# Optimization experiments

Hardware: AMD Instinct MI355X
Metric: run time of the kernel (lower is better)

Reference implementation:

```python
import jax, jax.numpy as jnp
import numpy as np

DIM = 768
HEADS = 12
SCALE = DIM ** -0.5  # NOTE: module scales by full dim, not head dim


def setup_inputs() -> dict:
    key = jax.random.key(0)
    ks = jax.random.split(key, 5)
    B, N, C = 8, 1024, DIM
    x = jax.random.normal(ks[0], (B, N, C), dtype=jnp.float32)
    W_qkv = jax.random.normal(ks[1], (C, 3 * C), dtype=jnp.float32) * (C ** -0.5)
    b_qkv = jnp.zeros((3 * C,), dtype=jnp.float32)
    W_out = jax.random.normal(ks[2], (C, C), dtype=jnp.float32) * (C ** -0.5)
    b_out = jnp.zeros((C,), dtype=jnp.float32)
    return {"x": x, "W_qkv": W_qkv, "b_qkv": b_qkv, "W_out": W_out, "b_out": b_out}


def reference(x, W_qkv, b_qkv, W_out, b_out) -> jnp.ndarray:
    B, N, C = x.shape
    H, D = HEADS, C // HEADS
    qkv = x @ W_qkv + b_qkv                       # [B, N, 3C]
    q, k, v = jnp.split(qkv, 3, axis=-1)
    # [B, N, C] -> [B, H, N, D]
    q = q.reshape(B, N, H, D).transpose(0, 2, 1, 3)
    k = k.reshape(B, N, H, D).transpose(0, 2, 1, 3)
    v = v.reshape(B, N, H, D).transpose(0, 2, 1, 3)
    attn = jnp.einsum("bhnd,bhmd->bhnm", q, k) * SCALE
    attn = jax.nn.softmax(attn, axis=-1)
    out = jnp.einsum("bhnm,bhmd->bhnd", attn, v)   # [B, H, N, D]
    out = out.transpose(0, 2, 1, 3).reshape(B, N, C)
    return out @ W_out + b_out
```

## Files before the change

kernel.cpp:

```cpp
#include <hip/hip_runtime.h>
#include <hip/hip_bf16.h>

typedef __attribute__((ext_vector_type(4))) float f32x4;
typedef __attribute__((ext_vector_type(4))) unsigned u32x4;
typedef __attribute__((ext_vector_type(8))) short bf16x8;

#define SCALE_F 0.03608439182435161f
#define QSCALE  (0.03608439182435161f * 1.44269504088896f)

__device__ __forceinline__ unsigned short f2bf(float f) {
    union { float f; unsigned u; } v; v.f = f;
    return (unsigned short)((v.u + 0x7FFFu + ((v.u >> 16) & 1u)) >> 16);
}

__device__ __forceinline__ float fast_exp2(float x) {
#if __has_builtin(__builtin_amdgcn_exp2f)
    return __builtin_amdgcn_exp2f(x);
#else
    return exp2f(x);
#endif
}

__device__ __forceinline__ void gload_lds16(const void* g, void* l) {
    __builtin_amdgcn_global_load_lds(
        (const __attribute__((address_space(1))) unsigned int*)g,
        (__attribute__((address_space(3))) unsigned int*)l, 16, 0, 0);
}

__global__ __launch_bounds__(256) void xcvt_kernel(const float* __restrict__ X,
                                                   unsigned short* __restrict__ Xb,
                                                   int n8) {
    const int i = blockIdx.x * 256 + threadIdx.x;
    if (i < n8) {
        f32x4 a = *(const f32x4*)(X + (size_t)i * 8);
        f32x4 b = *(const f32x4*)(X + (size_t)i * 8 + 4);
        bf16x8 w;
#pragma unroll
        for (int j = 0; j < 4; ++j) { w[j] = (short)f2bf(a[j]); w[4 + j] = (short)f2bf(b[j]); }
        *(bf16x8*)(Xb + (size_t)i * 8) = w;
    }
}

__global__ __launch_bounds__(256) void wtrans_kernel(const float* __restrict__ W,
                                                     unsigned short* __restrict__ WT,
                                                     int R, int C) {
    __shared__ unsigned short T[64][68];
    const int t = threadIdx.x;
    const int r0 = blockIdx.y * 64, c0 = blockIdx.x * 64;
    {
        const int lr = t >> 4, lc = (t & 15) * 4;
#pragma unroll
        for (int p = 0; p < 4; ++p) {
            const float* s = W + (size_t)(r0 + lr + p * 16) * C + c0 + lc;
            f32x4 v = *(const f32x4*)s;
            unsigned short* d = &T[lr + p * 16][lc];
            d[0] = f2bf(v[0]); d[1] = f2bf(v[1]); d[2] = f2bf(v[2]); d[3] = f2bf(v[3]);
        }
    }
    __syncthreads();
    {
        const int oc = t >> 3, j0 = (t & 7) * 8;
#pragma unroll
        for (int p = 0; p < 2; ++p) {
            const int c = oc + p * 32;
            bf16x8 v;
#pragma unroll
            for (int j = 0; j < 8; ++j) v[j] = (short)T[j0 + j][c];
            *(bf16x8*)(WT + (size_t)(c0 + c) * R + r0 + j0) = v;
        }
    }
}

__global__ __launch_bounds__(256) void qkv_gemm_kernel(
    const unsigned short* __restrict__ Xb, const unsigned short* __restrict__ WT,
    const float* __restrict__ bias,
    unsigned short* __restrict__ Qw, unsigned short* __restrict__ Kw,
    unsigned short* __restrict__ VTw)
{
    __shared__ unsigned short Alds[128 * 32];
    __shared__ unsigned short Blds[128 * 32];

    const int t = threadIdx.x;
    const int lane = t & 63, wave = t >> 6;
    const int l15 = lane & 15, l4 = lane >> 4;
    const int m0 = blockIdx.x * 128, n0 = blockIdx.y * 128;
    const int wr = wave >> 1, wc = wave & 1;

    f32x4 acc[4][4];
#pragma unroll
    for (int m = 0; m < 4; ++m)
#pragma unroll
        for (int n = 0; n < 4; ++n) acc[m][n] = (f32x4){0.f, 0.f, 0.f, 0.f};

    for (int k0 = 0; k0 < 768; k0 += 32) {
#pragma unroll
        for (int c = 0; c < 2; ++c) {
            const int o = wave * 1024 + lane * 16 + c * 4096;
            const int row = o >> 6, cb = o & 63;
            gload_lds16((const char*)(Xb + (size_t)(m0 + row) * 768 + k0) + cb,
                        (char*)Alds + wave * 1024 + c * 4096);
            gload_lds16((const char*)(WT + (size_t)(n0 + row) * 768 + k0) + cb,
                        (char*)Blds + wave * 1024 + c * 4096);
        }
        __syncthreads();
        bf16x8 af[4], bfr[4];
#pragma unroll
        for (int m = 0; m < 4; ++m)
            af[m] = *(const bf16x8*)((const char*)Alds + (wr * 64 + m * 16 + l15) * 64 + l4 * 16);
#pragma unroll
        for (int n = 0; n < 4; ++n)
            bfr[n] = *(const bf16x8*)((const char*)Blds + (wc * 64 + n * 16 + l15) * 64 + l4 * 16);
#pragma unroll
        for (int m = 0; m < 4; ++m)
#pragma unroll
            for (int n = 0; n < 4; ++n)
                acc[m][n] = __builtin_amdgcn_mfma_f32_16x16x32_bf16(af[m], bfr[n], acc[m][n], 0, 0, 0);
        __syncthreads();
    }

#pragma unroll
    for (int n = 0; n < 4; ++n) {
        const int col = n0 + wc * 64 + n * 16 + l15;
        const float bv = bias[col];
        const int which = col / 768;
        const int cc = col - which * 768;
        const int h = cc >> 6, dd = cc & 63;
#pragma unroll
        for (int m = 0; m < 4; ++m) {
#pragma unroll
            for (int r = 0; r < 4; ++r) {
                const int row = m0 + wr * 64 + m * 16 + l4 * 4 + r;
                const int b = row >> 10, ntok = row & 1023;
                const size_t bh = (size_t)b * 12 + h;
                float val = acc[m][n][r] + bv;
                if (which == 0) val *= QSCALE;
                const unsigned short hv = f2bf(val);
                if (which == 0)      Qw[(bh * 1024 + ntok) * 64 + dd] = hv;
                else if (which == 1) Kw[(bh * 1024 + ntok) * 64 + dd] = hv;
                else                 VTw[(bh * 64 + dd) * 1024 + ntok] = hv;
            }
        }
    }
}

__global__ __launch_bounds__(256) void attn_kernel(
    const unsigned short* __restrict__ Qw, const unsigned short* __restrict__ Kw,
    const unsigned short* __restrict__ VTw, unsigned short* __restrict__ A2)
{
    __shared__ unsigned short Klds[2 * 64 * 64];
    __shared__ unsigned short Vlds[2 * 64 * 64];
    __shared__ float Flds[4 * 16];

    const int t = threadIdx.x, lane = t & 63, wave = t >> 6;
    const int l15 = lane & 15, l4 = lane >> 4;
    const int wg = (blockIdx.x & 7) * 192 + (blockIdx.x >> 3);
    const int qt = wg & 15, bh = wg >> 4;
    const int q0 = qt * 64;

    const size_t kvbase = (size_t)bh * 1024 * 64;
    const size_t vtbase = (size_t)bh * 64 * 1024;

    const unsigned short* qptr = Qw + kvbase + (size_t)(q0 + wave * 16 + l15) * 64;
    const bf16x8 qf0 = *(const bf16x8*)((const char*)qptr + l4 * 16);
    const bf16x8 qf1 = *(const bf16x8*)((const char*)qptr + 64 + l4 * 16);

    f32x4 oacc[4];
#pragma unroll
    for (int d = 0; d < 4; ++d) oacc[d] = (f32x4){0.f, 0.f, 0.f, 0.f};
    float m_run = -1e30f, l_run = 0.f;

    auto STAGE = [&](int kt, int bufi) {
        const int kv0 = kt * 64;
        char* kb = (char*)Klds + bufi * 8192;
        char* vb = (char*)Vlds + bufi * 8192;
#pragma unroll
        for (int c = 0; c < 2; ++c) {
            const int oo = wave * 1024 + lane * 16 + c * 4096;
            const int R = oo >> 7, w = oo & 127;
            const int sw = w ^ ((R & 7) << 4);
            const int kvs = (R & 0x23) | ((R & 0x0C) << 1) | ((R & 0x10) >> 2);
            gload_lds16((const char*)(Kw + kvbase + (size_t)(kv0 + kvs) * 64) + sw,
                        kb + wave * 1024 + c * 4096);
            gload_lds16((const char*)(VTw + vtbase + (size_t)R * 1024 + kv0) + sw,
                        vb + wave * 1024 + c * 4096);
        }
    };

    STAGE(0, 0);
    for (int kt = 0; kt < 16; ++kt) {
        const int cur = kt & 1;
        if (kt < 15) {
            STAGE(kt + 1, cur ^ 1);
            asm volatile("s_waitcnt vmcnt(4)" ::: "memory");
        } else {
            asm volatile("s_waitcnt vmcnt(0)" ::: "memory");
        }
        __builtin_amdgcn_s_barrier();
        __builtin_amdgcn_sched_barrier(0);
        const char* kb = (const char*)Klds + cur * 8192;
        const char* vb = (const char*)Vlds + cur * 8192;

        f32x4 sacc[4];
#pragma unroll
        for (int i = 0; i < 4; ++i) sacc[i] = (f32x4){0.f, 0.f, 0.f, 0.f};
        __builtin_amdgcn_s_setprio(1);
#pragma unroll
        for (int ks = 0; ks < 2; ++ks) {
            const bf16x8 qq = ks ? qf1 : qf0;
#pragma unroll
            for (int kvf = 0; kvf < 4; ++kvf) {
                const int row = kvf * 16 + l15;
                int addr = row * 128 + ks * 64 + l4 * 16;
                addr ^= (row & 7) << 4;
                const bf16x8 kf = *(const bf16x8*)(kb + addr);
                sacc[kvf] = __builtin_amdgcn_mfma_f32_16x16x32_bf16(kf, qq, sacc[kvf], 0, 0, 0);
            }
        }
        __builtin_amdgcn_s_setprio(0);

        float p[16];
        float tmax = -1e30f;
#pragma unroll
        for (int i = 0; i < 4; ++i)
#pragma unroll
            for (int r = 0; r < 4; ++r) {
                p[i * 4 + r] = sacc[i][r];
                tmax = fmaxf(tmax, sacc[i][r]);
            }
        tmax = fmaxf(tmax, __shfl_xor(tmax, 16));
        tmax = fmaxf(tmax, __shfl_xor(tmax, 32));

        if (!__all(tmax - m_run <= 8.f)) {
            const float mnew = fmaxf(m_run, tmax);
            const float alpha = fast_exp2(m_run - mnew);
            m_run = mnew;
            if (lane < 16) Flds[wave * 16 + lane] = alpha;
            const f32x4 av = *(const f32x4*)(&Flds[wave * 16 + l4 * 4]);
#pragma unroll
            for (int d = 0; d < 4; ++d)
#pragma unroll
                for (int r = 0; r < 4; ++r) oacc[d][r] *= av[r];
            l_run *= alpha;
        }

        float tsum = 0.f;
#pragma unroll
        for (int i = 0; i < 16; ++i) { p[i] = fast_exp2(p[i] - m_run); tsum += p[i]; }
        tsum += __shfl_xor(tsum, 16);
        tsum += __shfl_xor(tsum, 32);
        l_run += tsum;

        bf16x8 paf[2];
#pragma unroll
        for (int ks = 0; ks < 2; ++ks) {
            union { u32x4 u; bf16x8 h; } cv;
#pragma unroll
            for (int j2 = 0; j2 < 4; ++j2)
                asm("v_cvt_pk_bf16_f32 %0, %1, %2"
                    : "=v"(cv.u[j2]) : "v"(p[ks * 8 + 2 * j2]), "v"(p[ks * 8 + 2 * j2 + 1]));
            paf[ks] = cv.h;
        }

        __builtin_amdgcn_s_setprio(1);
#pragma unroll
        for (int ks = 0; ks < 2; ++ks) {
#pragma unroll
            for (int df = 0; df < 4; ++df) {
                const int d = df * 16 + l15;
                int addr = d * 128 + ks * 64 + l4 * 16;
                addr ^= (d & 7) << 4;
                const bf16x8 vf = *(const bf16x8*)(vb + addr);
                oacc[df] = __builtin_amdgcn_mfma_f32_16x16x32_bf16(paf[ks], vf, oacc[df], 0, 0, 0);
            }
        }
        __builtin_amdgcn_s_setprio(0);
        __builtin_amdgcn_s_barrier();
    }

    if (lane < 16) Flds[wave * 16 + lane] = 1.f / l_run;
    const f32x4 inv = *(const f32x4*)(&Flds[wave * 16 + l4 * 4]);
    const int b = bh / 12, h = bh - b * 12;
#pragma unroll
    for (int df = 0; df < 4; ++df) {
#pragma unroll
        for (int r = 0; r < 4; ++r) {
            const int row = b * 1024 + q0 + wave * 16 + l4 * 4 + r;
            const int col = h * 64 + df * 16 + l15;
            A2[(size_t)row * 768 + col] = f2bf(oacc[df][r] * inv[r]);
        }
    }
}

__global__ __launch_bounds__(256) void out_gemm_kernel(
    const unsigned short* __restrict__ A2, const unsigned short* __restrict__ WT,
    const float* __restrict__ bias, float* __restrict__ Out)
{
    __shared__ unsigned short Alds[128 * 32];
    __shared__ unsigned short Blds[64 * 32];

    const int t = threadIdx.x;
    const int lane = t & 63, wave = t >> 6;
    const int l15 = lane & 15, l4 = lane >> 4;
    const int m0 = blockIdx.x * 128, n0 = blockIdx.y * 64;
    const int wr = wave >> 1, wc = wave & 1;

    f32x4 acc[4][2];
#pragma unroll
    for (int m = 0; m < 4; ++m)
#pragma unroll
        for (int n = 0; n < 2; ++n) acc[m][n] = (f32x4){0.f, 0.f, 0.f, 0.f};

    for (int k0 = 0; k0 < 768; k0 += 32) {
#pragma unroll
        for (int c = 0; c < 2; ++c) {
            const int o = wave * 1024 + lane * 16 + c * 4096;
            const int row = o >> 6, cb = o & 63;
            gload_lds16((const char*)(A2 + (size_t)(m0 + row) * 768 + k0) + cb,
                        (char*)Alds + wave * 1024 + c * 4096);
        }
        {
            const int o = t * 16;
            const int row = o >> 6, cb = o & 63;
            gload_lds16((const char*)(WT + (size_t)(n0 + row) * 768 + k0) + cb,
                        (char*)Blds + o);
        }
        __syncthreads();
        bf16x8 af[4], bfr[2];
#pragma unroll
        for (int m = 0; m < 4; ++m)
            af[m] = *(const bf16x8*)((const char*)Alds + (wr * 64 + m * 16 + l15) * 64 + l4 * 16);
#pragma unroll
        for (int n = 0; n < 2; ++n)
            bfr[n] = *(const bf16x8*)((const char*)Blds + (wc * 32 + n * 16 + l15) * 64 + l4 * 16);
#pragma unroll
        for (int m = 0; m < 4; ++m)
#pragma unroll
            for (int n = 0; n < 2; ++n)
                acc[m][n] = __builtin_amdgcn_mfma_f32_16x16x32_bf16(af[m], bfr[n], acc[m][n], 0, 0, 0);
        __syncthreads();
    }

#pragma unroll
    for (int n = 0; n < 2; ++n) {
        const int col = n0 + wc * 32 + n * 16 + l15;
        const float bv = bias[col];
#pragma unroll
        for (int m = 0; m < 4; ++m)
#pragma unroll
            for (int r = 0; r < 4; ++r) {
                const int row = m0 + wr * 64 + m * 16 + l4 * 4 + r;
                Out[(size_t)row * 768 + col] = acc[m][n][r] + bv;
            }
    }
}

extern "C" void kernel_launch(void* const* d_in, const int* in_sizes, int n_in,
                              void* d_out, int out_size, void* d_ws, size_t ws_size,
                              hipStream_t stream) {
    const float* X    = (const float*)d_in[0];
    const float* Wqkv = (const float*)d_in[1];
    const float* bqkv = (const float*)d_in[2];
    const float* Wout = (const float*)d_in[3];
    const float* bout = (const float*)d_in[4];
    float* Out = (float*)d_out;

    const size_t nq = (size_t)96 * 1024 * 64;
    unsigned short* XbA2  = (unsigned short*)d_ws;
    unsigned short* Qw    = XbA2 + nq;
    unsigned short* Kw    = Qw + nq;
    unsigned short* VTw   = Kw + nq;
    unsigned short* WqkvT = VTw + nq;
    unsigned short* WoutT = WqkvT + (size_t)2304 * 768;

    hipLaunchKernelGGL(xcvt_kernel, dim3(3072), dim3(256), 0, stream,
                       X, XbA2, 8192 * 768 / 8);
    hipLaunchKernelGGL(wtrans_kernel, dim3(36, 12), dim3(256), 0, stream,
                       Wqkv, WqkvT, 768, 2304);
    hipLaunchKernelGGL(wtrans_kernel, dim3(12, 12), dim3(256), 0, stream,
                       Wout, WoutT, 768, 768);
    hipLaunchKernelGGL(qkv_gemm_kernel, dim3(64, 18), dim3(256), 0, stream,
                       XbA2, WqkvT, bqkv, Qw, Kw, VTw);
    hipLaunchKernelGGL(attn_kernel, dim3(1536), dim3(256), 0, stream,
                       Qw, Kw, VTw, XbA2);
    hipLaunchKernelGGL(out_gemm_kernel, dim3(64, 12), dim3(256), 0, stream,
                       XbA2, WoutT, bout, Out);
}
```

Before: 137.7 us.

## Merge prep kernels, stage V transpose through LDS, double query rows per attention block

New measurement: 128.2 us. -6.9%, faster.

```diff
diff --git a/kernel.cpp b/kernel.cpp
--- a/kernel.cpp
+++ b/kernel.cpp
@@ -5,7 +5,6 @@
 typedef __attribute__((ext_vector_type(4))) unsigned u32x4;
 typedef __attribute__((ext_vector_type(8))) short bf16x8;
 
-#define SCALE_F 0.03608439182435161f
 #define QSCALE  (0.03608439182435161f * 1.44269504088896f)
 
 __device__ __forceinline__ unsigned short f2bf(float f) {
@@ -27,26 +26,30 @@
         (__attribute__((address_space(3))) unsigned int*)l, 16, 0, 0);
 }
 
-__global__ __launch_bounds__(256) void xcvt_kernel(const float* __restrict__ X,
-                                                   unsigned short* __restrict__ Xb,
-                                                   int n8) {
-    const int i = blockIdx.x * 256 + threadIdx.x;
-    if (i < n8) {
+__global__ __launch_bounds__(256) void prep_kernel(
+    const float* __restrict__ X, unsigned short* __restrict__ Xb,
+    const float* __restrict__ Wqkv, unsigned short* __restrict__ WqkvT,
+    const float* __restrict__ Wout, unsigned short* __restrict__ WoutT)
+{
+    __shared__ unsigned short T[64][68];
+    const int bid = blockIdx.x, t = threadIdx.x;
+
+    if (bid < 3072) {
+        const int i = bid * 256 + t;
         f32x4 a = *(const f32x4*)(X + (size_t)i * 8);
         f32x4 b = *(const f32x4*)(X + (size_t)i * 8 + 4);
         bf16x8 w;
 #pragma unroll
         for (int j = 0; j < 4; ++j) { w[j] = (short)f2bf(a[j]); w[4 + j] = (short)f2bf(b[j]); }
         *(bf16x8*)(Xb + (size_t)i * 8) = w;
-    }
-}
-
-__global__ __launch_bounds__(256) void wtrans_kernel(const float* __restrict__ W,
-                                                     unsigned short* __restrict__ WT,
-                                                     int R, int C) {
-    __shared__ unsigned short T[64][68];
-    const int t = threadIdx.x;
-    const int r0 = blockIdx.y * 64, c0 = blockIdx.x * 64;
+        return;
+    }
+
+    const float* W; unsigned short* WT; int C, bx, by;
+    if (bid < 3504) { W = Wqkv; WT = WqkvT; C = 2304; const int x = bid - 3072; bx = x % 36; by = x / 36; }
+    else            { W = Wout; WT = WoutT; C = 768;  const int x = bid - 3504; bx = x % 12; by = x / 12; }
+    const int R = 768;
+    const int r0 = by * 64, c0 = bx * 64;
     {
         const int lr = t >> 4, lc = (t & 15) * 4;
 #pragma unroll
@@ -77,8 +80,9 @@
     unsigned short* __restrict__ Qw, unsigned short* __restrict__ Kw,
     unsigned short* __restrict__ VTw)
 {
-    __shared__ unsigned short Alds[128 * 32];
-    __shared__ unsigned short Blds[128 * 32];
+    __shared__ unsigned short SMEM[64 * 136 + 64];
+    unsigned short* Alds = SMEM;
+    unsigned short* Blds = SMEM + 128 * 32;
 
     const int t = threadIdx.x;
     const int lane = t & 63, wave = t >> 6;
@@ -118,27 +122,61 @@
         __syncthreads();
     }
 
-#pragma unroll
-    for (int n = 0; n < 4; ++n) {
-        const int col = n0 + wc * 64 + n * 16 + l15;
-        const float bv = bias[col];
-        const int which = col / 768;
-        const int cc = col - which * 768;
-        const int h = cc >> 6, dd = cc & 63;
-#pragma unroll
-        for (int m = 0; m < 4; ++m) {
-#pragma unroll
-            for (int r = 0; r < 4; ++r) {
-                const int row = m0 + wr * 64 + m * 16 + l4 * 4 + r;
-                const int b = row >> 10, ntok = row & 1023;
-                const size_t bh = (size_t)b * 12 + h;
-                float val = acc[m][n][r] + bv;
-                if (which == 0) val *= QSCALE;
-                const unsigned short hv = f2bf(val);
-                if (which == 0)      Qw[(bh * 1024 + ntok) * 64 + dd] = hv;
-                else if (which == 1) Kw[(bh * 1024 + ntok) * 64 + dd] = hv;
-                else                 VTw[(bh * 64 + dd) * 1024 + ntok] = hv;
-            }
+    if (n0 < 1536) {
+        const int which = n0 / 768;
+#pragma unroll
+        for (int n = 0; n < 4; ++n) {
+            const int col = n0 + wc * 64 + n * 16 + l15;
+            const float bv = bias[col];
+            const int cc = col - which * 768;
+            const int h = cc >> 6, dd = cc & 63;
+#pragma unroll
+            for (int m = 0; m < 4; ++m) {
+#pragma unroll
+                for (int r = 0; r < 4; ++r) {
+                    const int row = m0 + wr * 64 + m * 16 + l4 * 4 + r;
+                    const int b = row >> 10, ntok = row & 1023;
+                    const size_t bh = (size_t)b * 12 + h;
+                    float val = acc[m][n][r] + bv;
+                    if (which == 0) val *= QSCALE;
+                    const unsigned short hv = f2bf(val);
+                    if (which == 0) Qw[(bh * 1024 + ntok) * 64 + dd] = hv;
+                    else            Kw[(bh * 1024 + ntok) * 64 + dd] = hv;
+                }
+            }
+        }
+    } else {
+        const int b = m0 >> 10, ntok0 = m0 & 1023;
+#pragma unroll
+        for (int chunk = 0; chunk < 2; ++chunk) {
+            if (wc == chunk) {
+#pragma unroll
+                for (int n = 0; n < 4; ++n) {
+                    const int cloc = n * 16 + l15;
+                    const float bv = bias[n0 + chunk * 64 + cloc];
+#pragma unroll
+                    for (int m = 0; m < 4; ++m)
+#pragma unroll
+                        for (int r = 0; r < 4; ++r) {
+                            const int ntl = wr * 64 + m * 16 + l4 * 4 + r;
+                            SMEM[cloc * 136 + ntl] = f2bf(acc[m][n][r] + bv);
+                        }
+                }
+            }
+            __syncthreads();
+            {
+                const int sub = t & 7;
+#pragma unroll
+                for (int rep = 0; rep < 2; ++rep) {
+                    const int cll = rep * 32 + (t >> 3);
+                    const int cc = n0 - 1536 + chunk * 64 + cll;
+                    const int h = cc >> 6, dd = cc & 63;
+                    const size_t rb = ((size_t)(b * 12 + h) * 64 + dd) * 1024 + ntok0 + sub * 8;
+                    *(bf16x8*)&VTw[rb]      = *(const bf16x8*)&SMEM[cll * 136 + sub * 8];
+                    *(bf16x8*)&VTw[rb + 64] = *(const bf16x8*)&SMEM[cll * 136 + 64 + sub * 8];
+                }
+            }
+            __syncthreads();
         }
     }
 }
@@ -149,25 +187,31 @@
 {
     __shared__ unsigned short Klds[2 * 64 * 64];
     __shared__ unsigned short Vlds[2 * 64 * 64];
-    __shared__ float Flds[4 * 16];
+    __shared__ float Flds[4 * 2 * 16];
 
     const int t = threadIdx.x, lane = t & 63, wave = t >> 6;
     const int l15 = lane & 15, l4 = lane >> 4;
-    const int wg = (blockIdx.x & 7) * 192 + (blockIdx.x >> 3);
-    const int qt = wg & 15, bh = wg >> 4;
-    const int q0 = qt * 64;
+    const int wg = (blockIdx.x & 7) * 96 + (blockIdx.x >> 3);
+    const int qt = wg & 7, bh = wg >> 3;
+    const int q0 = qt * 128;
 
     const size_t kvbase = (size_t)bh * 1024 * 64;
     const size_t vtbase = (size_t)bh * 64 * 1024;
 
-    const unsigned short* qptr = Qw + kvbase + (size_t)(q0 + wave * 16 + l15) * 64;
-    const bf16x8 qf0 = *(const bf16x8*)((const char*)qptr + l4 * 16);
-    const bf16x8 qf1 = *(const bf16x8*)((const char*)qptr + 64 + l4 * 16);
-
-    f32x4 oacc[4];
-#pragma unroll
-    for (int d = 0; d < 4; ++d) oacc[d] = (f32x4){0.f, 0.f, 0.f, 0.f};
-    float m_run = -1e30f, l_run = 0.f;
+    bf16x8 qf[2][2];
+#pragma unroll
+    for (int qs = 0; qs < 2; ++qs) {
+        const unsigned short* qptr = Qw + kvbase + (size_t)(q0 + qs * 64 + wave * 16 + l15) * 64;
+        qf[qs][0] = *(const bf16x8*)((const char*)qptr + l4 * 16);
+        qf[qs][1] = *(const bf16x8*)((const char*)qptr + 64 + l4 * 16);
+    }
+
+    f32x4 oacc[2][4];
+#pragma unroll
+    for (int qs = 0; qs < 2; ++qs)
+#pragma unroll
+        for (int d = 0; d < 4; ++d) oacc[qs][d] = (f32x4){0.f, 0.f, 0.f, 0.f};
+    float m_run[2] = {-1e30f, -1e30f}, l_run[2] = {0.f, 0.f};
 
     auto STAGE = [&](int kt, int bufi) {
         const int kv0 = kt * 64;
@@ -200,93 +244,99 @@
         const char* kb = (const char*)Klds + cur * 8192;
         const char* vb = (const char*)Vlds + cur * 8192;
 
-        f32x4 sacc[4];
-#pragma unroll
-        for (int i = 0; i < 4; ++i) sacc[i] = (f32x4){0.f, 0.f, 0.f, 0.f};
-        __builtin_amdgcn_s_setprio(1);
-#pragma unroll
-        for (int ks = 0; ks < 2; ++ks) {
-            const bf16x8 qq = ks ? qf1 : qf0;
-#pragma unroll
-            for (int kvf = 0; kvf < 4; ++kvf) {
-                const int row = kvf * 16 + l15;
-                int addr = row * 128 + ks * 64 + l4 * 16;
-                addr ^= (row & 7) << 4;
-                const bf16x8 kf = *(const bf16x8*)(kb + addr);
-                sacc[kvf] = __builtin_amdgcn_mfma_f32_16x16x32_bf16(kf, qq, sacc[kvf], 0, 0, 0);
-            }
-        }
-        __builtin_amdgcn_s_setprio(0);
-
-        float p[16];
-        float tmax = -1e30f;
-#pragma unroll
-        for (int i = 0; i < 4; ++i)
+#pragma unroll
+        for (int qs = 0; qs < 2; ++qs) {
+            f32x4 sacc[4];
+#pragma unroll
+            for (int i = 0; i < 4; ++i) sacc[i] = (f32x4){0.f, 0.f, 0.f, 0.f};
+            __builtin_amdgcn_s_setprio(1);
+#pragma unroll
+            for (int ks = 0; ks < 2; ++ks) {
+                const bf16x8 qq = qf[qs][ks];
+#pragma unroll
+                for (int kvf = 0; kvf < 4; ++kvf) {
+                    const int row = kvf * 16 + l15;
+                    int addr = row * 128 + ks * 64 + l4 * 16;
+                    addr ^= (row & 7) << 4;
+                    const bf16x8 kf = *(const bf16x8*)(kb + addr);
+                    sacc[kvf] = __builtin_amdgcn_mfma_f32_16x16x32_bf16(kf, qq, sacc[kvf], 0, 0, 0);
+                }
+            }
+            __builtin_amdgcn_s_setprio(0);
+
+            float p[16];
+            float tmax = -1e30f;
+#pragma unroll
+            for (int i = 0; i < 4; ++i)
+#pragma unroll
+                for (int r = 0; r < 4; ++r) {
+                    p[i * 4 + r] = sacc[i][r];
+                    tmax = fmaxf(tmax, sacc[i][r]);
+                }
+            tmax = fmaxf(tmax, __shfl_xor(tmax, 16));
+            tmax = fmaxf(tmax, __shfl_xor(tmax, 32));
+
+            if (!__all(tmax - m_run[qs] <= 8.f)) {
+                const float mnew = fmaxf(m_run[qs], tmax);
+                const float alpha = fast_exp2(m_run[qs] - mnew);
+                m_run[qs] = mnew;
+                if (lane < 16) Flds[wave * 32 + qs * 16 + lane] = alpha;
+                const f32x4 av = *(const f32x4*)(&Flds[wave * 32 + qs * 16 + l4 * 4]);
+#pragma unroll
+                for (int d = 0; d < 4; ++d)
+#pragma unroll
+                    for (int r = 0; r < 4; ++r) oacc[qs][d][r] *= av[r];
+                l_run[qs] *= alpha;
+            }
+
+            float tsum = 0.f;
+#pragma unroll
+            for (int i = 0; i < 16; ++i) { p[i] = fast_exp2(p[i] - m_run[qs]); tsum += p[i]; }
+            tsum += __shfl_xor(tsum, 16);
+            tsum += __shfl_xor(tsum, 32);
+            l_run[qs] += tsum;
+
+            bf16x8 paf[2];
+#pragma unroll
+            for (int ks = 0; ks < 2; ++ks) {
+                union { u32x4 u; bf16x8 h; } cv;
+#pragma unroll
+                for (int j2 = 0; j2 < 4; ++j2)
+                    asm("v_cvt_pk_bf16_f32 %0, %1, %2"
+                        : "=v"(cv.u[j2]) : "v"(p[ks * 8 + 2 * j2]), "v"(p[ks * 8 + 2 * j2 + 1]));
+                paf[ks] = cv.h;
+            }
+
+            __builtin_amdgcn_s_setprio(1);
+#pragma unroll
+            for (int ks = 0; ks < 2; ++ks) {
+#pragma unroll
+                for (int df = 0; df < 4; ++df) {
+                    const int d = df * 16 + l15;
+                    int addr = d * 128 + ks * 64 + l4 * 16;
+                    addr ^= (d & 7) << 4;
+                    const bf16x8 vf = *(const bf16x8*)(vb + addr);
+                    oacc[qs][df] = __builtin_amdgcn_mfma_f32_16x16x32_bf16(paf[ks], vf, oacc[qs][df], 0, 0, 0);
+                }
+            }
+            __builtin_amdgcn_s_setprio(0);
+        }
+        __builtin_amdgcn_s_barrier();
+    }
+
+    const int b = bh / 12, h = bh - b * 12;
+#pragma unroll
+    for (int qs = 0; qs < 2; ++qs) {
+        if (lane < 16) Flds[wave * 32 + qs * 16 + lane] = 1.f / l_run[qs];
+        const f32x4 inv = *(const f32x4*)(&Flds[wave * 32 + qs * 16 + l4 * 4]);
+#pragma unroll
+        for (int df = 0; df < 4; ++df) {
 #pragma unroll
             for (int r = 0; r < 4; ++r) {
-                p[i * 4 + r] = sacc[i][r];
-                tmax = fmaxf(tmax, sacc[i][r]);
-            }
-        tmax = fmaxf(tmax, __shfl_xor(tmax, 16));
-        tmax = fmaxf(tmax, __shfl_xor(tmax, 32));
-
-        if (!__all(tmax - m_run <= 8.f)) {
-            const float mnew = fmaxf(m_run, tmax);
-            const float alpha = fast_exp2(m_run - mnew);
-            m_run = mnew;
-            if (lane < 16) Flds[wave * 16 + lane] = alpha;
-            const f32x4 av = *(const f32x4*)(&Flds[wave * 16 + l4 * 4]);
-#pragma unroll
-            for (int d = 0; d < 4; ++d)
-#pragma unroll
-                for (int r = 0; r < 4; ++r) oacc[d][r] *= av[r];
-            l_run *= alpha;
-        }
-
-        float tsum = 0.f;
-#pragma unroll
-        for (int i = 0; i < 16; ++i) { p[i] = fast_exp2(p[i] - m_run); tsum += p[i]; }
-        tsum += __shfl_xor(tsum, 16);
-        tsum += __shfl_xor(tsum, 32);
-        l_run += tsum;
-
-        bf16x8 paf[2];
-#pragma unroll
-        for (int ks = 0; ks < 2; ++ks) {
-            union { u32x4 u; bf16x8 h; } cv;
-#pragma unroll
-            for (int j2 = 0; j2 < 4; ++j2)
-                asm("v_cvt_pk_bf16_f32 %0, %1, %2"
-                    : "=v"(cv.u[j2]) : "v"(p[ks * 8 + 2 * j2]), "v"(p[ks * 8 + 2 * j2 + 1]));
-            paf[ks] = cv.h;
-        }
-
-        __builtin_amdgcn_s_setprio(1);
-#pragma unroll
-        for (int ks = 0; ks < 2; ++ks) {
-#pragma unroll
-            for (int df = 0; df < 4; ++df) {
-                const int d = df * 16 + l15;
-                int addr = d * 128 + ks * 64 + l4 * 16;
-                addr ^= (d & 7) << 4;
-                const bf16x8 vf = *(const bf16x8*)(vb + addr);
-                oacc[df] = __builtin_amdgcn_mfma_f32_16x16x32_bf16(paf[ks], vf, oacc[df], 0, 0, 0);
-            }
-        }
-        __builtin_amdgcn_s_setprio(0);
-        __builtin_amdgcn_s_barrier();
-    }
-
-    if (lane < 16) Flds[wave * 16 + lane] = 1.f / l_run;
-    const f32x4 inv = *(const f32x4*)(&Flds[wave * 16 + l4 * 4]);
-    const int b = bh / 12, h = bh - b * 12;
-#pragma unroll
-    for (int df = 0; df < 4; ++df) {
-#pragma unroll
-        for (int r = 0; r < 4; ++r) {
-            const int row = b * 1024 + q0 + wave * 16 + l4 * 4 + r;
-            const int col = h * 64 + df * 16 + l15;
-            A2[(size_t)row * 768 + col] = f2bf(oacc[df][r] * inv[r]);
+                const int row = b * 1024 + q0 + qs * 64 + wave * 16 + l4 * 4 + r;
+                const int col = h * 64 + df * 16 + l15;
+                A2[(size_t)row * 768 + col] = f2bf(oacc[qs][df][r] * inv[r]);
+            }
         }
     }
 }
@@ -372,15 +422,11 @@
     unsigned short* WqkvT = VTw + nq;
     unsigned short* WoutT = WqkvT + (size_t)2304 * 768;
 
-    hipLaunchKernelGGL(xcvt_kernel, dim3(3072), dim3(256), 0, stream,
-                       X, XbA2, 8192 * 768 / 8);
-    hipLaunchKernelGGL(wtrans_kernel, dim3(36, 12), dim3(256), 0, stream,
-                       Wqkv, WqkvT, 768, 2304);
-    hipLaunchKernelGGL(wtrans_kernel, dim3(12, 12), dim3(256), 0, stream,
-                       Wout, WoutT, 768, 768);
+    hipLaunchKernelGGL(prep_kernel, dim3(3648), dim3(256), 0, stream,
+                       X, XbA2, Wqkv, WqkvT, Wout, WoutT);
     hipLaunchKernelGGL(qkv_gemm_kernel, dim3(64, 18), dim3(256), 0, stream,
                        XbA2, WqkvT, bqkv, Qw, Kw, VTw);
-    hipLaunchKernelGGL(attn_kernel, dim3(1536), dim3(256), 0, stream,
+    hipLaunchKernelGGL(attn_kernel, dim3(768), dim3(256), 0, stream,
                        Qw, Kw, VTw, XbA2);
     hipLaunchKernelGGL(out_gemm_kernel, dim3(64, 12), dim3(256), 0, stream,
                        XbA2, WoutT, bout, Out);
```
